# Performance work log

Measured on AMD Instinct MI355X. Metric: run time of the kernel, lower is better.

The kernel has to match this reference:

```python
import jax, jax.numpy as jnp
import numpy as np
from jax import lax

H, MEM, AUX = 1024, 256, 16
S = MEM + AUX          # total_slots
B, T = 8, 4096
TOPK = 8               # top_k_binding
GAMMA, BETA, PTS = 0.92, 0.08, 0.4  # gamma, beta, prediction_torque_scale
RANK = 10              # coupling_rank == prediction_rank


def _inv_softplus(v):
    return float(np.log(np.expm1(max(float(v), 1e-6))))


def setup_inputs() -> dict:
    key = jax.random.key(0)
    ks = jax.random.split(key, 8)
    x = jax.random.normal(ks[0], (B, T, H), dtype=jnp.float32)
    # base basis: orthonormal columns in the first MEM slots (memory_dim < hidden_dim -> QR branch)
    q, _ = jnp.linalg.qr(jax.random.normal(ks[1], (H, MEM), dtype=jnp.float32))
    basis = jnp.zeros((H, S), jnp.float32).at[:, :MEM].set(q)
    return dict(
        x=x,
        basis=basis,
        tape_init_re=jax.random.normal(ks[2], (S,), dtype=jnp.float32) / S ** 0.5,
        tape_init_im=jax.random.normal(ks[3], (S,), dtype=jnp.float32) / S ** 0.5,
        eta_raw=jnp.asarray(_inv_softplus(0.08), jnp.float32),
        alpha=jnp.asarray(0.35, jnp.float32),
        torque_rotation=jnp.zeros((S,), jnp.float32),
        w_r=jnp.zeros((S,), jnp.float32),
        breadth_gate=jnp.zeros((S,), jnp.float32),
        epsilon_factor=jax.random.normal(ks[4], (S, RANK), dtype=jnp.float32) * 0.02,
        epsilon_scale=jnp.zeros((RANK,), jnp.float32),
        epsilon_diag=jnp.zeros((S,), jnp.float32),
        pred_factor=jax.random.normal(ks[5], (S, RANK), dtype=jnp.float32) * 0.02,
        pred_scale=jnp.zeros((RANK,), jnp.float32),
        pred_diag=jnp.zeros((S,), jnp.float32),
    )


def _forward(x, basis, tape_init_re, tape_init_im, eta_raw, alpha,
             torque_rotation, w_r, breadth_gate,
             epsilon_factor, epsilon_scale, epsilon_diag,
             pred_factor, pred_scale, pred_diag):
    active = jnp.arange(S) < MEM                      # base slots active (fixed population)
    amf = active.astype(jnp.float32)
    eta = jax.nn.softplus(eta_raw)
    # low-rank Hermitian coupling epsilon and prediction operator W_pred
    eps = (epsilon_factor * epsilon_scale) @ epsilon_factor.T + jnp.diag(epsilon_diag)
    wp = (pred_factor * pred_scale) @ pred_factor.T + jnp.diag(pred_diag)
    eps_c = eps.astype(jnp.complex64)
    wp_c = wp.astype(jnp.complex64)
    rot = jnp.exp(1j * torque_rotation.astype(jnp.complex64))  # torque phase rotation
    wr_gate = jax.nn.sigmoid(w_r)
    bg = jax.nn.sigmoid(breadth_gate)

    def renorm(tape):
        masked = tape * amf
        nrm = jnp.sqrt(jnp.maximum((jnp.abs(masked) ** 2).sum(-1, keepdims=True), 1e-16))
        return masked / nrm

    tape0 = (tape_init_re + 1j * tape_init_im) * amf   # aux slots zeroed as in _complex_tape_init
    tape0 = renorm(jnp.broadcast_to(tape0, (B, S)))

    def step(carry, x_t):
        tape, prev = carry                              # [B,S] complex64 each
        m = jnp.einsum('hs,bh->bs', basis, x_t)         # project into slot space
        mag = jnp.abs(m) * amf
        kth = lax.top_k(mag, TOPK)[0][:, -1:]           # top-k binding threshold
        inj = jnp.where((mag >= kth) & active, m, 0.0).astype(jnp.complex64)
        rotated = tape * rot
        drive = jnp.einsum('st,bt->bs', eps_c, rotated)  # coupling drive
        pred = jnp.einsum('st,bt->bs', wp_c, rotated)    # prediction torque
        new = (GAMMA * rotated + eta * drive + BETA * inj
               + PTS * 1j * pred + wr_gate * prev)
        new = renorm(new)
        y = x_t + alpha * jnp.einsum('hs,bs->bh', basis, bg * new.real)
        return (new, tape), y

    (_, _), ys = lax.scan(step, (tape0, tape0), jnp.swapaxes(x, 0, 1))
    return jnp.swapaxes(ys, 0, 1)


def reference(x, basis, tape_init_re, tape_init_im, eta_raw, alpha,
              torque_rotation, w_r, breadth_gate,
              epsilon_factor, epsilon_scale, epsilon_diag,
              pred_factor, pred_scale, pred_diag):
    return _forward(x, basis, tape_init_re, tape_init_im, eta_raw, alpha,
                    torque_rotation, w_r, breadth_gate,
                    epsilon_factor, epsilon_scale, epsilon_diag,
                    pred_factor, pred_scale, pred_diag)
```

## Files before the change

kernel.cpp:

```cpp
#include <hip/hip_runtime.h>
#include <cstdint>
#include <cstddef>

#define HD    1024
#define SLOTS 272
#define MEMS  256
#define BATCH 8
#define TT    4096
#define RR    (BATCH*TT)
#define RANKC 10

#define GAMMA 0.92f
#define BETA  0.08f
#define PTS   0.4f

typedef float f32x2 __attribute__((ext_vector_type(2)));
typedef float f32x4 __attribute__((ext_vector_type(4)));
typedef short bf16x8 __attribute__((ext_vector_type(8)));
#define PKFMA(a, b, c) __builtin_elementwise_fma((a), (b), (c))

#define DPP_ADD(v, ctrl, rmask)                                                   \
    v += __int_as_float(__builtin_amdgcn_update_dpp(                              \
        0, __float_as_int(v), (ctrl), (rmask), 0xf, true))

__device__ __forceinline__ float wave_sum_bcast(float v)
{
    DPP_ADD(v, 0xB1,  0xf);
    DPP_ADD(v, 0x4E,  0xf);
    DPP_ADD(v, 0x141, 0xf);
    DPP_ADD(v, 0x140, 0xf);
    DPP_ADD(v, 0x142, 0xa);
    DPP_ADD(v, 0x143, 0xc);
    return __int_as_float(__builtin_amdgcn_readlane(__float_as_int(v), 63));
}

__device__ __forceinline__ unsigned short f2bf(float f)
{
    unsigned u = __float_as_uint(f);
    u = (u + 0x7FFFu + ((u >> 16) & 1u)) >> 16;
    return (unsigned short)u;
}

__global__ void prep_kernel(const float* __restrict__ t0re, const float* __restrict__ t0im,
                            const float* __restrict__ eta_raw,
                            const float* __restrict__ trot, const float* __restrict__ w_r,
                            const float* __restrict__ bgate,
                            const float* __restrict__ eps_scale, const float* __restrict__ pred_scale,
                            const float* __restrict__ eps_diag, const float* __restrict__ pred_diag,
                            float* __restrict__ consts, int* __restrict__ flags)
{
    __shared__ float red[MEMS];
    const int s = threadIdx.x;
    const float tr = t0re[s], ti = t0im[s];
    red[s] = tr * tr + ti * ti;
    __syncthreads();
    for (int off = 128; off > 0; off >>= 1) {
        if (s < off) red[s] += red[s + off];
        __syncthreads();
    }
    const float nrm = sqrtf(fmaxf(red[0], 1e-16f));
    const float eta = log1pf(expf(eta_raw[0]));
    const float rc = cosf(trot[s]), rs = sinf(trot[s]);
    const float c1 = GAMMA + eta * eps_diag[s];
    const float c2 = PTS * pred_diag[s];
    consts[0 * MEMS + s] = 1.0f / (1.0f + expf(-w_r[s]));
    consts[1 * MEMS + s] = 1.0f / (1.0f + expf(-bgate[s]));
    consts[2 * MEMS + s] = c1 * rc - c2 * rs;
    consts[3 * MEMS + s] = c1 * rs + c2 * rc;
    consts[4 * MEMS + s] = tr / nrm;
    consts[5 * MEMS + s] = ti / nrm;
    consts[6 * MEMS + s] = rc;
    consts[7 * MEMS + s] = rs;
    if (s == 0) {
        consts[8 * MEMS] = eta;
        int f1 = 0, f2 = 0;
        for (int k = 0; k < RANKC; ++k) {
            if (eps_scale[k]  != 0.0f) f1 = 1;
            if (pred_scale[k] != 0.0f) f2 = 1;
        }
        flags[0] = f1;
        flags[1] = f2;
    }
}

__global__ void gprep_kernel(const float* __restrict__ basis,
                             const float* __restrict__ alpha_p,
                             const float* __restrict__ consts,
                             unsigned short* __restrict__ G)
{
    const int h = blockIdx.x;
    const int k = threadIdx.x;
    const float g = alpha_p[0] * consts[MEMS + k] * basis[(size_t)h * SLOTS + k];
    G[(size_t)h * MEMS + k] = f2bf(g);
}

__global__ __launch_bounds__(256) void proj_topk_kernel(const float* __restrict__ x,
                                                        const float* __restrict__ basis,
                                                        float* __restrict__ M)
{
    __shared__ float pAs[16][64];
    __shared__ float pBs[16][260];
    const int tid  = threadIdx.x;
    const size_t row0 = (size_t)blockIdx.x * 64;
    const int mt = tid >> 5;
    const int nt = tid & 31;
    const int ar = tid >> 2;
    const int ak = (tid & 3) * 4;
    const int bk = tid >> 4;
    const int bn = (tid & 15) * 16;
    float acc[2][2][4][4] = {};
    for (int k0 = 0; k0 < HD; k0 += 16) {
        {
            const float4 av = *(const float4*)&x[(row0 + ar) * HD + k0 + ak];
            pAs[ak + 0][ar] = av.x; pAs[ak + 1][ar] = av.y;
            pAs[ak + 2][ar] = av.z; pAs[ak + 3][ar] = av.w;
#pragma unroll
            for (int c = 0; c < 4; ++c) {
                const float4 bv = *(const float4*)&basis[(size_t)(k0 + bk) * SLOTS + bn + c * 4];
                *(float4*)&pBs[bk][bn + c * 4] = bv;
            }
        }
        __syncthreads();
#pragma unroll
        for (int kk = 0; kk < 16; ++kk) {
            const float4 a0 = *(const float4*)&pAs[kk][mt * 4];
            const float4 a1 = *(const float4*)&pAs[kk][32 + mt * 4];
            const float4 b0 = *(const float4*)&pBs[kk][nt * 4];
            const float4 b1 = *(const float4*)&pBs[kk][128 + nt * 4];
            const float av[2][4] = {{a0.x, a0.y, a0.z, a0.w}, {a1.x, a1.y, a1.z, a1.w}};
            const float bv[2][4] = {{b0.x, b0.y, b0.z, b0.w}, {b1.x, b1.y, b1.z, b1.w}};
#pragma unroll
            for (int p = 0; p < 2; ++p)
#pragma unroll
                for (int q = 0; q < 2; ++q)
#pragma unroll
                    for (int i = 0; i < 4; ++i)
#pragma unroll
                        for (int j = 0; j < 4; ++j)
                            acc[p][q][i][j] += av[p][i] * bv[q][j];
        }
        __syncthreads();
    }
#pragma unroll
    for (int p = 0; p < 2; ++p)
#pragma unroll
        for (int i = 0; i < 4; ++i) {
            float v[8], a[8], w8[8];
#pragma unroll
            for (int q = 0; q < 2; ++q)
#pragma unroll
                for (int j = 0; j < 4; ++j) {
                    v[q * 4 + j] = acc[p][q][i][j];
                    a[q * 4 + j] = fabsf(v[q * 4 + j]);
                    w8[q * 4 + j] = a[q * 4 + j];
                }
            float kv = 0.0f;
#pragma unroll
            for (int it = 0; it < 8; ++it) {
                float lm = w8[0]; int li = 0;
#pragma unroll
                for (int e = 1; e < 8; ++e)
                    if (w8[e] > lm) { lm = w8[e]; li = e; }
                float bm = lm; int bi = nt * 8 + li;
#pragma unroll
                for (int off = 1; off < 32; off <<= 1) {
                    float om = __shfl_xor(bm, off);
                    int   oi = __shfl_xor(bi, off);
                    if (om > bm || (om == bm && oi < bi)) { bm = om; bi = oi; }
                }
                kv = bm;
                if ((bi >> 3) == nt) w8[bi & 7] = -1.0f;
            }
            const int r = p * 32 + mt * 4 + i;
#pragma unroll
            for (int q = 0; q < 2; ++q) {
                float4 o;
                o.x = (a[q * 4 + 0] >= kv) ? BETA * v[q * 4 + 0] : 0.0f;
                o.y = (a[q * 4 + 1] >= kv) ? BETA * v[q * 4 + 1] : 0.0f;
                o.z = (a[q * 4 + 2] >= kv) ? BETA * v[q * 4 + 2] : 0.0f;
                o.w = (a[q * 4 + 3] >= kv) ? BETA * v[q * 4 + 3] : 0.0f;
                *(float4*)&M[(row0 + r) * MEMS + q * 128 + nt * 4] = o;
            }
        }
}

__global__ __launch_bounds__(64) void scan_kernel(const float* __restrict__ M,
                                                  const float* __restrict__ consts,
                                                  const int* __restrict__ flags,
                                                  const float* __restrict__ eps_fac,
                                                  const float* __restrict__ eps_scale,
                                                  const float* __restrict__ eps_diag,
                                                  const float* __restrict__ pred_fac,
                                                  const float* __restrict__ pred_scale,
                                                  const float* __restrict__ pred_diag,
                                                  float* __restrict__ Wout)
{
    const int b    = blockIdx.x;
    const int lane = threadIdx.x;
    const int s0   = lane * 4;
    const int general = flags[0] | flags[1];
    const size_t base = (size_t)b * TT * MEMS + s0;

    if (!general) {
        f32x2 wrg[2], A2[2], B2[2];
        f32x2 wre[2], wim[2], qre[2], qim[2];
        {
            const float4 w4 = *(const float4*)&consts[0 * MEMS + s0];
            const float4 a4 = *(const float4*)&consts[2 * MEMS + s0];
            const float4 b4 = *(const float4*)&consts[3 * MEMS + s0];
            const float4 r4 = *(const float4*)&consts[4 * MEMS + s0];
            const float4 i4 = *(const float4*)&consts[5 * MEMS + s0];
            wrg[0] = {w4.x, w4.y};  wrg[1] = {w4.z, w4.w};
            A2[0]  = {a4.x, a4.y};  A2[1]  = {a4.z, a4.w};
            B2[0]  = {b4.x, b4.y};  B2[1]  = {b4.z, b4.w};
            wre[0] = {r4.x, r4.y};  wre[1] = {r4.z, r4.w};
            wim[0] = {i4.x, i4.y};  wim[1] = {i4.z, i4.w};
            qre[0] = wre[0]; qre[1] = wre[1];
            qim[0] = wim[0]; qim[1] = wim[1];
        }
        float ssp;
        {
            const f32x2 p0 = PKFMA(wim[0], wim[0], wre[0] * wre[0]);
            const f32x2 p1 = PKFMA(wim[1], wim[1], wre[1] * wre[1]);
            const f32x2 pp = p0 + p1;
            ssp = pp.x + pp.y;
        }
        float4 mbuf[16];
#pragma unroll
        for (int j = 0; j < 16; ++j)
            mbuf[j] = *(const float4*)&M[base + (size_t)j * MEMS];
        for (int t0 = 0; t0 < TT; t0 += 16) {
#pragma unroll
            for (int j = 0; j < 16; ++j) {
                const int t = t0 + j;
                const float4 mc = mbuf[j];
                mbuf[j] = *(const float4*)&M[base + (size_t)(t + 16) * MEMS];
                const float stot = wave_sum_bcast(ssp);
                const float icv  = __builtin_amdgcn_rsqf(fmaxf(stot, 1e-16f));
                const f32x2 ic2  = {icv, icv};
                const f32x2 Lr0 = PKFMA(A2[0], wre[0], -(B2[0] * wim[0]));
                const f32x2 Li0 = PKFMA(B2[0], wre[0],  A2[0] * wim[0]);
                const f32x2 Lr1 = PKFMA(A2[1], wre[1], -(B2[1] * wim[1]));
                const f32x2 Li1 = PKFMA(B2[1], wre[1],  A2[1] * wim[1]);
                const f32x2 m0 = {mc.x, mc.y};
                const f32x2 m1 = {mc.z, mc.w};
                const f32x2 Wr0 = PKFMA(wrg[0], qre[0], m0);
                const f32x2 Wi0 = wrg[0] * qim[0];
                const f32x2 Wr1 = PKFMA(wrg[1], qre[1], m1);
                const f32x2 Wi1 = wrg[1] * qim[1];
                const f32x2 u1r0 = PKFMA(ic2, Lr0, Wr0);
                const f32x2 u1i0 = PKFMA(ic2, Li0, Wi0);
                const f32x2 u1r1 = PKFMA(ic2, Lr1, Wr1);
                const f32x2 u1i1 = PKFMA(ic2, Li1, Wi1);
                const f32x2 ps0 = PKFMA(u1i0, u1i0, u1r0 * u1r0);
                const f32x2 ps1 = PKFMA(u1i1, u1i1, u1r1 * u1r1);
                const f32x2 pp  = ps0 + ps1;
                const f32x2 nr0 = wre[0] * ic2, ni0 = wim[0] * ic2;
                const f32x2 nr1 = wre[1] * ic2, ni1 = wim[1] * ic2;
                const int trow = t ? (t - 1) : 0;
                const float4 st4 = {nr0.x, nr0.y, nr1.x, nr1.y};
                *(float4*)&Wout[base + (size_t)trow * MEMS] = st4;
                qre[0] = nr0;  qim[0] = ni0;  qre[1] = nr1;  qim[1] = ni1;
                wre[0] = u1r0; wim[0] = u1i0; wre[1] = u1r1; wim[1] = u1i1;
                ssp = pp.x + pp.y;
            }
        }
        {
            const float stot = wave_sum_bcast(ssp);
            const float icv  = __builtin_amdgcn_rsqf(fmaxf(stot, 1e-16f));
            const float4 wq4 = {wre[0].x * icv, wre[0].y * icv,
                                wre[1].x * icv, wre[1].y * icv};
            *(float4*)&Wout[base + (size_t)(TT - 1) * MEMS] = wq4;
        }
        return;
    }

    float wr4[4], ur[4], ui[4], pr[4], pi[4];
    float rc4[4], rs4[4], ed4[4], pd4[4];
#pragma unroll
    for (int i = 0; i < 4; ++i) {
        wr4[i] = consts[0 * MEMS + s0 + i];
        ur[i]  = consts[4 * MEMS + s0 + i];
        ui[i]  = consts[5 * MEMS + s0 + i];
        pr[i] = ur[i]; pi[i] = ui[i];
        rc4[i] = consts[6 * MEMS + s0 + i];
        rs4[i] = consts[7 * MEMS + s0 + i];
        ed4[i] = eps_diag[s0 + i];
        pd4[i] = pred_diag[s0 + i];
    }
    const float eta  = consts[8 * MEMS];
    const int es_any = flags[0];
    const int ps_any = flags[1];
    float4 mbuf[4];
#pragma unroll
    for (int j = 0; j < 4; ++j)
        mbuf[j] = *(const float4*)&M[base + (size_t)j * MEMS];
    for (int t0 = 0; t0 < TT; t0 += 4) {
#pragma unroll
        for (int j = 0; j < 4; ++j) {
            const int t = t0 + j;
            const float4 mc = mbuf[j];
            const int pft = (t + 4 < TT) ? (t + 4) : (TT - 1);
            mbuf[j] = *(const float4*)&M[base + (size_t)pft * MEMS];
            float rr[4], ri[4], nr[4], ni[4];
#pragma unroll
            for (int i = 0; i < 4; ++i) {
                rr[i] = ur[i] * rc4[i] - ui[i] * rs4[i];
                ri[i] = ur[i] * rs4[i] + ui[i] * rc4[i];
            }
            const float mv[4] = {mc.x, mc.y, mc.z, mc.w};
#pragma unroll
            for (int i = 0; i < 4; ++i) {
                nr[i] = GAMMA * rr[i] + wr4[i] * pr[i] + eta * ed4[i] * rr[i]
                        - PTS * pd4[i] * ri[i] + mv[i];
                ni[i] = GAMMA * ri[i] + wr4[i] * pi[i] + eta * ed4[i] * ri[i]
                        + PTS * pd4[i] * rr[i];
            }
            if (es_any) {
#pragma unroll
                for (int k = 0; k < RANKC; ++k) {
                    float u[4], prj = 0.0f, pij = 0.0f;
#pragma unroll
                    for (int i = 0; i < 4; ++i) {
                        u[i] = eps_fac[(size_t)(s0 + i) * RANKC + k];
                        prj = fmaf(u[i], rr[i], prj);
                        pij = fmaf(u[i], ri[i], pij);
                    }
                    prj = wave_sum_bcast(prj);
                    pij = wave_sum_bcast(pij);
                    const float sc = eta * eps_scale[k];
#pragma unroll
                    for (int i = 0; i < 4; ++i) {
                        nr[i] = fmaf(sc * u[i], prj, nr[i]);
                        ni[i] = fmaf(sc * u[i], pij, ni[i]);
                    }
                }
            }
            if (ps_any) {
#pragma unroll
                for (int k = 0; k < RANKC; ++k) {
                    float u[4], qrj = 0.0f, qij = 0.0f;
#pragma unroll
                    for (int i = 0; i < 4; ++i) {
                        u[i] = pred_fac[(size_t)(s0 + i) * RANKC + k];
                        qrj = fmaf(u[i], rr[i], qrj);
                        qij = fmaf(u[i], ri[i], qij);
                    }
                    qrj = wave_sum_bcast(qrj);
                    qij = wave_sum_bcast(qij);
                    const float sc = PTS * pred_scale[k];
#pragma unroll
                    for (int i = 0; i < 4; ++i) {
                        nr[i] = fmaf(-sc * u[i], qij, nr[i]);
                        ni[i] = fmaf( sc * u[i], qrj, ni[i]);
                    }
                }
            }
            float ss = 0.0f;
#pragma unroll
            for (int i = 0; i < 4; ++i) ss = fmaf(nr[i], nr[i], fmaf(ni[i], ni[i], ss));
            ss = wave_sum_bcast(ss);
            const float inv = __builtin_amdgcn_rsqf(fmaxf(ss, 1e-16f));
#pragma unroll
            for (int i = 0; i < 4; ++i) {
                pr[i] = ur[i]; pi[i] = ui[i];
                ur[i] = nr[i] * inv; ui[i] = ni[i] * inv;
            }
            const float4 wq = {ur[0], ur[1], ur[2], ur[3]};
            *(float4*)&Wout[base + (size_t)t * MEMS] = wq;
        }
    }
}

__global__ __launch_bounds__(256) void outp_kernel(const float* __restrict__ W,
                                                   const unsigned short* __restrict__ G,
                                                   const float* __restrict__ x,
                                                   float* __restrict__ y)
{
    const int tid = threadIdx.x;
    const int w   = tid >> 6;
    const int l   = tid & 63;
    const int ln  = l & 15;
    const int lk  = (l >> 4) * 8;
    const size_t row0 = (size_t)blockIdx.x * 64 + (size_t)w * 16;
    const int col0 = blockIdx.y * 256;

    bf16x8 af[8];
    {
        const float* wrow = &W[(row0 + ln) * MEMS];
#pragma unroll
        for (int c = 0; c < 8; ++c) {
            const float4 a0 = *(const float4*)&wrow[c * 32 + lk];
            const float4 a1 = *(const float4*)&wrow[c * 32 + lk + 4];
            bf16x8 f;
            f[0] = (short)f2bf(a0.x); f[1] = (short)f2bf(a0.y);
            f[2] = (short)f2bf(a0.z); f[3] = (short)f2bf(a0.w);
            f[4] = (short)f2bf(a1.x); f[5] = (short)f2bf(a1.y);
            f[6] = (short)f2bf(a1.z); f[7] = (short)f2bf(a1.w);
            af[c] = f;
        }
    }
#pragma unroll
    for (int ct = 0; ct < 16; ++ct) {
        const int h = col0 + ct * 16 + ln;
        const unsigned short* grow = &G[(size_t)h * MEMS + lk];
        f32x4 acc = {0.0f, 0.0f, 0.0f, 0.0f};
#pragma unroll
        for (int c = 0; c < 8; ++c) {
            const bf16x8 bf = *(const bf16x8*)&grow[c * 32];
            acc = __builtin_amdgcn_mfma_f32_16x16x32_bf16(af[c], bf, acc, 0, 0, 0);
        }
        const size_t rbase = (row0 + (size_t)((l >> 4) * 4)) * HD + h;
#pragma unroll
        for (int i = 0; i < 4; ++i) {
            const size_t ro = rbase + (size_t)i * HD;
            y[ro] = x[ro] + acc[i];
        }
    }
}

extern "C" void kernel_launch(void* const* d_in, const int* in_sizes, int n_in,
                              void* d_out, int out_size, void* d_ws, size_t ws_size,
                              hipStream_t stream)
{
    const float* x          = (const float*)d_in[0];
    const float* basis      = (const float*)d_in[1];
    const float* t0re       = (const float*)d_in[2];
    const float* t0im       = (const float*)d_in[3];
    const float* eta_raw    = (const float*)d_in[4];
    const float* alpha      = (const float*)d_in[5];
    const float* trot       = (const float*)d_in[6];
    const float* w_r        = (const float*)d_in[7];
    const float* bgate      = (const float*)d_in[8];
    const float* eps_fac    = (const float*)d_in[9];
    const float* eps_scale  = (const float*)d_in[10];
    const float* eps_diag   = (const float*)d_in[11];
    const float* pred_fac   = (const float*)d_in[12];
    const float* pred_scale = (const float*)d_in[13];
    const float* pred_diag  = (const float*)d_in[14];
    float* out = (float*)d_out;

    const size_t szM = (size_t)RR * MEMS * sizeof(float);
    const size_t szW = szM;
    const size_t szC = 16384;
    const size_t szG = (size_t)HD * MEMS * 2;

    char* ws = (char*)d_ws;
    float *Mbuf, *Wbuf, *cbuf;
    unsigned short* Gbuf;
    if (ws_size >= szM + szW + szC + szG) {
        Mbuf = (float*)(ws);
        Wbuf = (float*)(ws + szM);
        cbuf = (float*)(ws + szM + szW);
        Gbuf = (unsigned short*)(ws + szM + szW + szC);
    } else {
        Mbuf = (float*)d_out;
        Wbuf = (float*)(ws);
        cbuf = (float*)(ws + szW);
        Gbuf = (unsigned short*)(ws + szW + szC);
    }
    int* fbuf = (int*)(cbuf + 8 * MEMS + 16);

    prep_kernel<<<1, 256, 0, stream>>>(t0re, t0im, eta_raw, trot, w_r, bgate,
                                       eps_scale, pred_scale, eps_diag, pred_diag,
                                       cbuf, fbuf);
    gprep_kernel<<<HD, 256, 0, stream>>>(basis, alpha, cbuf, Gbuf);
    proj_topk_kernel<<<RR / 64, 256, 0, stream>>>(x, basis, Mbuf);
    scan_kernel<<<BATCH, 64, 0, stream>>>(Mbuf, cbuf, fbuf,
                                          eps_fac, eps_scale, eps_diag,
                                          pred_fac, pred_scale, pred_diag,
                                          Wbuf);
    outp_kernel<<<dim3(RR / 64, HD / 256), 256, 0, stream>>>(Wbuf, Gbuf, x, out);
}
```

Measured before the change: 991.5 us.

## Run projection GEMM on bf16 MFMA with split hi/lo (bf16x3) precision

Replaces the fp32 SIMT tiled GEMM in the projection/top-k kernel with bf16 MFMA 16x16x32 instructions. Operands are split into high and low bf16 parts and three products are summed to keep near-fp32 accuracy for the top-k threshold. A new prep kernel pre-transposes and splits the basis into Qh/Ql buffers in workspace. The rewritten kernel drops LDS staging and loads B fragments straight from global memory. The risks are extra global traffic and MFMA work from the three products, and slight top-k tie changes from rounding.

```diff
diff --git a/kernel.cpp b/kernel.cpp
--- a/kernel.cpp
+++ b/kernel.cpp
@@ -39,6 +39,10 @@
     unsigned u = __float_as_uint(f);
     u = (u + 0x7FFFu + ((u >> 16) & 1u)) >> 16;
     return (unsigned short)u;
+}
+__device__ __forceinline__ float bf2f(unsigned short h)
+{
+    return __uint_as_float((unsigned)h << 16);
 }
 
 __global__ void prep_kernel(const float* __restrict__ t0re, const float* __restrict__ t0im,
@@ -94,94 +98,98 @@
     G[(size_t)h * MEMS + k] = f2bf(g);
 }
 
+__global__ void qprep_kernel(const float* __restrict__ basis,
+                             unsigned short* __restrict__ Qh,
+                             unsigned short* __restrict__ Ql)
+{
+    const int n = blockIdx.x;
+    for (int k = threadIdx.x; k < HD; k += 256) {
+        const float q = basis[(size_t)k * SLOTS + n];
+        const unsigned short h = f2bf(q);
+        Qh[(size_t)n * HD + k] = h;
+        Ql[(size_t)n * HD + k] = f2bf(q - bf2f(h));
+    }
+}
+
 __global__ __launch_bounds__(256) void proj_topk_kernel(const float* __restrict__ x,
-                                                        const float* __restrict__ basis,
+                                                        const unsigned short* __restrict__ Qh,
+                                                        const unsigned short* __restrict__ Ql,
                                                         float* __restrict__ M)
 {
-    __shared__ float pAs[16][64];
-    __shared__ float pBs[16][260];
-    const int tid  = threadIdx.x;
-    const size_t row0 = (size_t)blockIdx.x * 64;
-    const int mt = tid >> 5;
-    const int nt = tid & 31;
-    const int ar = tid >> 2;
-    const int ak = (tid & 3) * 4;
-    const int bk = tid >> 4;
-    const int bn = (tid & 15) * 16;
-    float acc[2][2][4][4] = {};
-    for (int k0 = 0; k0 < HD; k0 += 16) {
+    const int tid = threadIdx.x;
+    const int w   = tid >> 6;
+    const int l   = tid & 63;
+    const int ln  = l & 15;
+    const int lk  = (l >> 4) * 8;
+    const size_t row0 = (size_t)blockIdx.x * 64 + (size_t)w * 16;
+
+    f32x4 acc[16] = {};
+    for (int kb = 0; kb < HD; kb += 128) {
+        bf16x8 ah[4], al[4];
         {
-            const float4 av = *(const float4*)&x[(row0 + ar) * HD + k0 + ak];
-            pAs[ak + 0][ar] = av.x; pAs[ak + 1][ar] = av.y;
-            pAs[ak + 2][ar] = av.z; pAs[ak + 3][ar] = av.w;
+            const float* xr = &x[(row0 + ln) * HD + kb + lk];
 #pragma unroll
             for (int c = 0; c < 4; ++c) {
-                const float4 bv = *(const float4*)&basis[(size_t)(k0 + bk) * SLOTS + bn + c * 4];
-                *(float4*)&pBs[bk][bn + c * 4] = bv;
-            }
-        }
-        __syncthreads();
-#pragma unroll
-        for (int kk = 0; kk < 16; ++kk) {
-            const float4 a0 = *(const float4*)&pAs[kk][mt * 4];
-            const float4 a1 = *(const float4*)&pAs[kk][32 + mt * 4];
-            const float4 b0 = *(const float4*)&pBs[kk][nt * 4];
-            const float4 b1 = *(const float4*)&pBs[kk][128 + nt * 4];
-            const float av[2][4] = {{a0.x, a0.y, a0.z, a0.w}, {a1.x, a1.y, a1.z, a1.w}};
-            const float bv[2][4] = {{b0.x, b0.y, b0.z, b0.w}, {b1.x, b1.y, b1.z, b1.w}};
-#pragma unroll
-            for (int p = 0; p < 2; ++p)
-#pragma unroll
-                for (int q = 0; q < 2; ++q)
-#pragma unroll
-                    for (int i = 0; i < 4; ++i)
-#pragma unroll
-                        for (int j = 0; j < 4; ++j)
-                            acc[p][q][i][j] += av[p][i] * bv[q][j];
-        }
-        __syncthreads();
-    }
-#pragma unroll
-    for (int p = 0; p < 2; ++p)
-#pragma unroll
-        for (int i = 0; i < 4; ++i) {
-            float v[8], a[8], w8[8];
-#pragma unroll
-            for (int q = 0; q < 2; ++q)
-#pragma unroll
-                for (int j = 0; j < 4; ++j) {
-                    v[q * 4 + j] = acc[p][q][i][j];
-                    a[q * 4 + j] = fabsf(v[q * 4 + j]);
-                    w8[q * 4 + j] = a[q * 4 + j];
+                const float4 a0 = *(const float4*)&xr[c * 32];
+                const float4 a1 = *(const float4*)&xr[c * 32 + 4];
+                const float av[8] = {a0.x, a0.y, a0.z, a0.w, a1.x, a1.y, a1.z, a1.w};
+                bf16x8 h, lo;
+#pragma unroll
+                for (int j = 0; j < 8; ++j) {
+                    const unsigned short hb = f2bf(av[j]);
+                    h[j]  = (short)hb;
+                    lo[j] = (short)f2bf(av[j] - bf2f(hb));
                 }
-            float kv = 0.0f;
-#pragma unroll
-            for (int it = 0; it < 8; ++it) {
-                float lm = w8[0]; int li = 0;
-#pragma unroll
-                for (int e = 1; e < 8; ++e)
-                    if (w8[e] > lm) { lm = w8[e]; li = e; }
-                float bm = lm; int bi = nt * 8 + li;
-#pragma unroll
-                for (int off = 1; off < 32; off <<= 1) {
-                    float om = __shfl_xor(bm, off);
-                    int   oi = __shfl_xor(bi, off);
-                    if (om > bm || (om == bm && oi < bi)) { bm = om; bi = oi; }
-                }
-                kv = bm;
-                if ((bi >> 3) == nt) w8[bi & 7] = -1.0f;
-            }
-            const int r = p * 32 + mt * 4 + i;
-#pragma unroll
-            for (int q = 0; q < 2; ++q) {
-                float4 o;
-                o.x = (a[q * 4 + 0] >= kv) ? BETA * v[q * 4 + 0] : 0.0f;
-                o.y = (a[q * 4 + 1] >= kv) ? BETA * v[q * 4 + 1] : 0.0f;
-                o.z = (a[q * 4 + 2] >= kv) ? BETA * v[q * 4 + 2] : 0.0f;
-                o.w = (a[q * 4 + 3] >= kv) ? BETA * v[q * 4 + 3] : 0.0f;
-                *(float4*)&M[(row0 + r) * MEMS + q * 128 + nt * 4] = o;
-            }
-        }
+                ah[c] = h; al[c] = lo;
+            }
+        }
+#pragma unroll
+        for (int ct = 0; ct < 16; ++ct) {
+            const unsigned short* qhp = &Qh[(size_t)(ct * 16 + ln) * HD + kb + lk];
+            const unsigned short* qlp = &Ql[(size_t)(ct * 16 + ln) * HD + kb + lk];
+            f32x4 a = acc[ct];
+#pragma unroll
+            for (int c = 0; c < 4; ++c) {
+                const bf16x8 bh = *(const bf16x8*)&qhp[c * 32];
+                const bf16x8 bl = *(const bf16x8*)&qlp[c * 32];
+                a = __builtin_amdgcn_mfma_f32_16x16x32_bf16(ah[c], bh, a, 0, 0, 0);
+                a = __builtin_amdgcn_mfma_f32_16x16x32_bf16(al[c], bh, a, 0, 0, 0);
+                a = __builtin_amdgcn_mfma_f32_16x16x32_bf16(ah[c], bl, a, 0, 0, 0);
+            }
+            acc[ct] = a;
+        }
+    }
+#pragma unroll
+    for (int i = 0; i < 4; ++i) {
+        float v16[16], a16[16], w16[16];
+#pragma unroll
+        for (int ct = 0; ct < 16; ++ct) {
+            v16[ct] = acc[ct][i];
+            a16[ct] = fabsf(v16[ct]);
+            w16[ct] = a16[ct];
+        }
+        float kv = 0.0f;
+#pragma unroll
+        for (int it = 0; it < 8; ++it) {
+            float lm = w16[0]; int li = 0;
+#pragma unroll
+            for (int e = 1; e < 16; ++e)
+                if (w16[e] > lm) { lm = w16[e]; li = e; }
+            float bm = lm; int bi = ln * 16 + li;
+#pragma unroll
+            for (int off = 1; off < 16; off <<= 1) {
+                const float om = __shfl_xor(bm, off);
+                const int   oi = __shfl_xor(bi, off);
+                if (om > bm || (om == bm && oi < bi)) { bm = om; bi = oi; }
+            }
+            kv = bm;
+            if ((bi >> 4) == ln) w16[bi & 15] = -1.0f;
+        }
+        const size_t r = row0 + (size_t)((l >> 4) * 4 + i);
+#pragma unroll
+        for (int ct = 0; ct < 16; ++ct)
+            M[r * MEMS + ct * 16 + ln] = (a16[ct] >= kv) ? BETA * v16[ct] : 0.0f;
+    }
 }
 
 __global__ __launch_bounds__(64) void scan_kernel(const float* __restrict__ M,
@@ -444,20 +452,25 @@
     const size_t szW = szM;
     const size_t szC = 16384;
     const size_t szG = (size_t)HD * MEMS * 2;
+    const size_t szQ = (size_t)MEMS * HD * 2;
 
     char* ws = (char*)d_ws;
     float *Mbuf, *Wbuf, *cbuf;
-    unsigned short* Gbuf;
-    if (ws_size >= szM + szW + szC + szG) {
-        Mbuf = (float*)(ws);
-        Wbuf = (float*)(ws + szM);
-        cbuf = (float*)(ws + szM + szW);
-        Gbuf = (unsigned short*)(ws + szM + szW + szC);
+    unsigned short *Gbuf, *Qhbuf, *Qlbuf;
+    if (ws_size >= szM + szW + szC + szG + 2 * szQ) {
+        Mbuf  = (float*)(ws);
+        Wbuf  = (float*)(ws + szM);
+        cbuf  = (float*)(ws + szM + szW);
+        Gbuf  = (unsigned short*)(ws + szM + szW + szC);
+        Qhbuf = (unsigned short*)(ws + szM + szW + szC + szG);
+        Qlbuf = (unsigned short*)(ws + szM + szW + szC + szG + szQ);
     } else {
-        Mbuf = (float*)d_out;
-        Wbuf = (float*)(ws);
-        cbuf = (float*)(ws + szW);
-        Gbuf = (unsigned short*)(ws + szW + szC);
+        Mbuf  = (float*)d_out;
+        Wbuf  = (float*)(ws);
+        cbuf  = (float*)(ws + szW);
+        Gbuf  = (unsigned short*)(ws + szW + szC);
+        Qhbuf = (unsigned short*)(ws + szW + szC + szG);
+        Qlbuf = (unsigned short*)(ws + szW + szC + szG + szQ);
     }
     int* fbuf = (int*)(cbuf + 8 * MEMS + 16);
 
@@ -465,7 +478,8 @@
                                        eps_scale, pred_scale, eps_diag, pred_diag,
                                        cbuf, fbuf);
     gprep_kernel<<<HD, 256, 0, stream>>>(basis, alpha, cbuf, Gbuf);
-    proj_topk_kernel<<<RR / 64, 256, 0, stream>>>(x, basis, Mbuf);
+    qprep_kernel<<<MEMS, 256, 0, stream>>>(basis, Qhbuf, Qlbuf);
+    proj_topk_kernel<<<RR / 64, 256, 0, stream>>>(x, Qhbuf, Qlbuf, Mbuf);
     scan_kernel<<<BATCH, 64, 0, stream>>>(Mbuf, cbuf, fbuf,
                                           eps_fac, eps_scale, eps_diag,
                                           pred_fac, pred_scale, pred_diag,
```

New measurement: 1.029 ms. 3.8% more time.
